# Performance work log

Measured on AMD Instinct MI355X. Metric: run time of the kernel, lower is better.

## Reference

```python
import jax, jax.numpy as jnp
import numpy as np

ALPHA = 1.0
BETA = 0.5
B, N, T = 4096, 32, 8
EPS = 1e-8


def _lsa_square(cost):
    """Jonker-Volgenant shortest augmenting path LSA on a square cost [n,n].
    Returns col_of_row[i] = column assigned to row i (same as scipy's
    linear_sum_assignment col_ind for square matrices)."""
    n = cost.shape[0]
    INF = np.inf
    u = np.zeros(n + 1)
    v = np.zeros(n + 1)
    p = np.zeros(n + 1, dtype=np.int64)   # p[j] = row matched to column j (1-based)
    way = np.zeros(n + 1, dtype=np.int64)
    for i in range(1, n + 1):
        p[0] = i
        j0 = 0
        minv = np.full(n + 1, INF)
        used = np.zeros(n + 1, dtype=bool)
        while True:
            used[j0] = True
            i0 = p[j0]
            # vectorized relaxation over all unused columns
            cur = cost[i0 - 1] - u[i0] - v[1:]
            free = ~used[1:]
            mv = minv[1:]
            wy = way[1:]
            upd = free & (cur < mv)
            mv[upd] = cur[upd]
            wy[upd] = j0
            masked = np.where(free, mv, INF)
            j1 = int(np.argmin(masked)) + 1
            delta = masked[j1 - 1]
            u[p[used]] += delta
            v[used] -= delta
            minv[~used] -= delta
            j0 = j1
            if p[j0] == 0:
                break
        while j0:
            j1 = way[j0]
            p[j0] = p[j1]
            j0 = j1
    col_of_row = np.empty(n, dtype=np.int32)
    for j in range(1, n + 1):
        col_of_row[p[j] - 1] = j - 1
    return col_of_row


def _batched_lsa(cost):
    cost = np.asarray(cost, dtype=np.float64)
    return np.stack([_lsa_square(c) for c in cost]).astype(np.int32)


def hungarian(cost):
    b, n = cost.shape[0], cost.shape[1]
    return jax.pure_callback(_batched_lsa, jax.ShapeDtypeStruct((b, n), jnp.int32), cost)


def _assignment(pred_j, logits, target_j, target_types):
    # j_cost[b,i,j] = |pred_j[b,i] - target_j[b,j]|
    j_cost = jnp.abs(pred_j[:, :, None] - target_j[:, None, :])
    # torch code uses -log(softmax + 1e-8) for the cost matrix (not log_softmax)
    logp = jnp.log(jax.nn.softmax(logits, axis=-1) + EPS)      # [B,N,T]
    idx = jnp.broadcast_to(target_types[:, None, :].astype(jnp.int32), j_cost.shape)
    type_cost = -jnp.take_along_axis(logp, idx, axis=-1)       # [B,N,N]
    cost = ALPHA * j_cost + BETA * type_cost
    return hungarian(jax.lax.stop_gradient(cost))              # [B,N] int32


def _matched_loss(pred_j, logits, target_j, target_types, cols):
    # row_ind == arange(N) for square full-mask case; cols = assigned targets
    tj = jnp.take_along_axis(target_j, cols.astype(jnp.int32), axis=1)        # [B,N]
    tt = jnp.take_along_axis(target_types, cols.astype(jnp.int64), axis=1)    # [B,N]
    j_loss = jnp.abs(pred_j - tj).sum()
    ls = jax.nn.log_softmax(logits, axis=-1)
    type_loss = -jnp.take_along_axis(ls, tt[..., None].astype(jnp.int32), axis=-1).sum()
    total = pred_j.shape[0] * pred_j.shape[1]
    loss = (ALPHA * j_loss + BETA * type_loss) / total
    j_mae = j_loss / total
    type_acc = (jnp.argmax(logits, axis=-1) == tt).astype(jnp.float32).mean()
    return loss, j_mae, type_acc


def setup_inputs() -> dict:
    key = jax.random.key(0)
    k1, k2, k3, k4 = jax.random.split(key, 4)
    return {
        'pred_j': jax.random.normal(k1, (B, N), dtype=jnp.float32),
        'pred_type_logits': jax.random.normal(k2, (B, N, T), dtype=jnp.float32),
        'target_j': jax.random.normal(k3, (B, N), dtype=jnp.float32),
        'target_types': jax.random.randint(k4, (B, N), 0, T, dtype=jnp.int64),
        'pred_mask': jnp.ones((B, N), dtype=bool),
        'target_mask': jnp.ones((B, N), dtype=bool),
    }


def reference(pred_j, pred_type_logits, target_j, target_types, pred_mask, target_mask):
    # Masks are all-ones here, so every slot is valid and the per-sample
    # torch loop vectorizes into one batched computation (same math).
    cols = _assignment(pred_j, pred_type_logits, target_j, target_types)
    loss, j_mae, type_acc = _matched_loss(pred_j, pred_type_logits, target_j, target_types, cols)
    return loss, j_mae, type_acc
```

## Files before the change

kernel.cpp:

```cpp
#include <hip/hip_runtime.h>
#include <math.h>


constexpr int BB = 4096;
constexpr int NN = 32;
constexpr int TT = 8;
constexpr float ALPHA_F = 1.0f;
constexpr float BETA_F  = 0.5f;
constexpr float EPS_F   = 1e-8f;

typedef float f32x32 __attribute__((ext_vector_type(32)));

template <int CTRL, int ROW_MASK>
__device__ __forceinline__ float dpp_min(float x) {
    int t = __builtin_amdgcn_update_dpp(__float_as_int(x), __float_as_int(x),
                                        CTRL, ROW_MASK, 0xf, false);
    return fminf(x, __int_as_float(t));
}

__device__ __forceinline__ float wave32_min_bcast(float x) {
    x = dpp_min<0xB1,  0xf>(x);
    x = dpp_min<0x4E,  0xf>(x);
    x = dpp_min<0x124, 0xf>(x);
    x = dpp_min<0x128, 0xf>(x);
    x = dpp_min<0x142, 0xa>(x);
    return __int_as_float(__builtin_amdgcn_readlane(__float_as_int(x), 31));
}

__device__ __forceinline__ float readlane_f(float x, int lane) {
    return __int_as_float(__builtin_amdgcn_readlane(__float_as_int(x), lane));
}

__global__ __launch_bounds__(256) void hungarian_lsa_kernel(
    const float* __restrict__ pred_j,
    const float* __restrict__ logits,
    const float* __restrict__ target_j,
    const int*   __restrict__ target_types,
    double* __restrict__ partials)
{
    __shared__ float lgpS[4][NN * TT];
    __shared__ float lgtS[4][NN * TT];

    const int wave = threadIdx.x >> 6;
    const int lane = threadIdx.x & 63;
    const int col  = lane & 31;
    const int b    = blockIdx.x * 4 + wave;

    float* lgp = lgpS[wave];
    float* lgt = lgtS[wave];

    const float pj = pred_j  [b * NN + col];
    const float tj = target_j[b * NN + col];
    const int   tt = target_types[b * NN + col];

    float x[TT];
    const float* lrow = logits + ((size_t)b * NN + col) * TT;
#pragma unroll
    for (int t = 0; t < TT; ++t) x[t] = lrow[t];

    float m = x[0]; int am = 0;
#pragma unroll
    for (int t = 1; t < TT; ++t) { if (x[t] > m) { m = x[t]; am = t; } }
    float s = 0.f;
#pragma unroll
    for (int t = 0; t < TT; ++t) s += expf(x[t] - m);
    const float lse = m + logf(s);

    if (lane < 32) {
#pragma unroll
        for (int t = 0; t < TT; ++t) {
            float p = expf(x[t] - m) / s;
            lgp[col * TT + t] = logf(p + EPS_F);
            lgt[col * TT + t] = x[t];
        }
    }
    __syncthreads();

    f32x32 cc;
#pragma unroll
    for (int r = 0; r < NN; ++r) {
        const float pjr = readlane_f(pj, r);
        const float lp  = lgp[r * TT + tt];
        cc[r] = ALPHA_F * fabsf(pjr - tj) + BETA_F * (-lp);
    }

    const float INFF = __builtin_inff();
    float v_f  = 0.0f;
    float uc_f = 0.0f;
    int   p_i  = 0;
    unsigned amask = 0;

    for (int i = 1; i <= NN; ++i) {
        bool used_b = false;

        float cur = cc[i - 1] - v_f;
        float mv  = wave32_min_bcast(cur);
        unsigned long long bm = __ballot(cur == mv);
        int   j1      = __ffsll(bm);
        float rowSum  = mv;

        while ((amask >> (j1 - 1)) & 1u) {
            const int j0 = j1;
            used_b |= (col == j0 - 1);
            const int   r0    = __builtin_amdgcn_readlane(p_i, j0 - 1) - 1;
            const float uc_j0 = readlane_f(uc_f, j0 - 1);
            const float cur2  = cc[r0] - v_f;
            const float curm  = used_b ? INFF : cur2;
            mv = wave32_min_bcast(curm);
            bm = __ballot((!used_b) && (cur2 == mv));
            j1 = __ffsll(bm);
            const float delta = mv - uc_j0;
            rowSum += delta;
            if (used_b) { v_f -= delta; uc_f += delta; }
        }

        if (col == j1 - 1) { p_i = i; uc_f = rowSum; }
        amask |= 1u << (j1 - 1);
    }

    const int   row      = p_i - 1;
    const float pj_row   = __shfl(pj,  row);
    const float lse_row  = __shfl(lse, row);
    const int   am_row   = __shfl(am,  row);
    const float logit_tt = lgt[row * TT + tt];

    double sj = (lane < 32) ? (double)fabsf(pj_row - tj)   : 0.0;
    double st = (lane < 32) ? (double)(lse_row - logit_tt) : 0.0;
    double sa = (lane < 32) ? ((am_row == tt) ? 1.0 : 0.0) : 0.0;
#pragma unroll
    for (int off = 32; off >= 1; off >>= 1) {
        sj += __shfl_xor(sj, off);
        st += __shfl_xor(st, off);
        sa += __shfl_xor(sa, off);
    }
    if (lane == 0) {
        partials[b * 3 + 0] = sj;
        partials[b * 3 + 1] = st;
        partials[b * 3 + 2] = sa;
    }
}

__global__ __launch_bounds__(256) void hungarian_finalize_kernel(
    const double* __restrict__ partials, float* __restrict__ out)
{
    __shared__ double sm0[256], sm1[256], sm2[256];
    const int tid = threadIdx.x;
    double a = 0.0, c = 0.0, e = 0.0;
    for (int i = tid; i < BB; i += 256) {
        a += partials[i * 3 + 0];
        c += partials[i * 3 + 1];
        e += partials[i * 3 + 2];
    }
    sm0[tid] = a; sm1[tid] = c; sm2[tid] = e;
    __syncthreads();
    for (int s = 128; s > 0; s >>= 1) {
        if (tid < s) {
            sm0[tid] += sm0[tid + s];
            sm1[tid] += sm1[tid + s];
            sm2[tid] += sm2[tid + s];
        }
        __syncthreads();
    }
    if (tid == 0) {
        const double jl = sm0[0], tl = sm1[0], ac = sm2[0];
        const double total = (double)BB * (double)NN;
        out[0] = (float)((jl + 0.5 * tl) / total);
        out[1] = (float)(jl / total);
        out[2] = (float)(ac / total);
    }
}

extern "C" void kernel_launch(void* const* d_in, const int* in_sizes, int n_in,
                              void* d_out, int out_size, void* d_ws, size_t ws_size,
                              hipStream_t stream) {
    const float* pred_j       = (const float*)d_in[0];
    const float* logits       = (const float*)d_in[1];
    const float* target_j     = (const float*)d_in[2];
    const int*   target_types = (const int*)  d_in[3];

    double* partials = (double*)d_ws;
    float*  out      = (float*)d_out;

    hungarian_lsa_kernel<<<BB / 4, 256, 0, stream>>>(
        pred_j, logits, target_j, target_types, partials);
    hungarian_finalize_kernel<<<1, 256, 0, stream>>>(partials, out);
}
```

Baseline: 49.87 us.

## Flatten Hungarian augment loops into single loop with lazy dual updates

Restructures the nested row/augmenting-path loops of the per-wave shortest augmenting path solver into one flat loop. Per-column dual updates are deferred: each visited column snapshots the running row sum, and the potential corrections are applied once when the row is assigned, instead of updating v and u on every step. Used columns are masked by adding infinity rather than by select-and-compare. This removes per-iteration dual updates and extra branches, at the cost of subtle float-rounding differences and a more intricate state machine that could alter tie-breaking.

```diff
diff --git a/kernel.cpp b/kernel.cpp
--- a/kernel.cpp
+++ b/kernel.cpp
@@ -85,40 +85,47 @@
     }
 
     const float INFF = __builtin_inff();
-    float v_f  = 0.0f;
-    float uc_f = 0.0f;
-    int   p_i  = 0;
-    unsigned amask = 0;
+    float negv  = 0.f;
+    float vmask = 0.f;
+    float ucf   = 0.f;
+    float snap  = 0.f;
+    float rowSum = 0.f;
+    float u_curV = 0.f;
+    int   p_m1  = 0;
+    unsigned amask = 0u;
+    int i  = 1;
+    int r0 = 0;
 
-    for (int i = 1; i <= NN; ++i) {
-        bool used_b = false;
+    for (;;) {
+        const float cur2 = cc[r0] + negv;
+        const float curm = cur2 + vmask;
+        const float mv   = wave32_min_bcast(curm);
+        const unsigned long long bm = __ballot(curm == mv);
+        const int   j1m1 = __ffsll(bm) - 1;
+        const float delta = mv - u_curV;
+        rowSum += delta;
+        const bool  isJ = (col == j1m1);
 
-        float cur = cc[i - 1] - v_f;
-        float mv  = wave32_min_bcast(cur);
-        unsigned long long bm = __ballot(cur == mv);
-        int   j1      = __ffsll(bm);
-        float rowSum  = mv;
-
-        while ((amask >> (j1 - 1)) & 1u) {
-            const int j0 = j1;
-            used_b |= (col == j0 - 1);
-            const int   r0    = __builtin_amdgcn_readlane(p_i, j0 - 1) - 1;
-            const float uc_j0 = readlane_f(uc_f, j0 - 1);
-            const float cur2  = cc[r0] - v_f;
-            const float curm  = used_b ? INFF : cur2;
-            mv = wave32_min_bcast(curm);
-            bm = __ballot((!used_b) && (cur2 == mv));
-            j1 = __ffsll(bm);
-            const float delta = mv - uc_j0;
-            rowSum += delta;
-            if (used_b) { v_f -= delta; uc_f += delta; }
+        if ((amask >> j1m1) & 1u) {
+            snap   = isJ ? rowSum : snap;
+            vmask  = isJ ? INFF   : vmask;
+            u_curV = readlane_f(ucf, j1m1);
+            r0     = __builtin_amdgcn_readlane(p_m1, j1m1);
+        } else {
+            p_m1 = isJ ? (i - 1) : p_m1;
+            const float dv  = rowSum - snap;
+            const float dvj = (vmask > 0.f) ? dv : 0.f;
+            negv += dvj;
+            ucf  += dvj;
+            ucf   = isJ ? rowSum : ucf;
+            amask |= 1u << j1m1;
+            if (i == NN) break;
+            ++i; r0 = i - 1;
+            vmask = 0.f; snap = 0.f; rowSum = 0.f; u_curV = 0.f;
         }
-
-        if (col == j1 - 1) { p_i = i; uc_f = rowSum; }
-        amask |= 1u << (j1 - 1);
     }
 
-    const int   row      = p_i - 1;
+    const int   row      = p_m1;
     const float pj_row   = __shfl(pj,  row);
     const float lse_row  = __shfl(lse, row);
     const int   am_row   = __shfl(am,  row);
```

After: 65.92 us. 32.2% more time.
